# Optimization experiments

Measured on AMD Instinct MI355X. Metric: run time of the kernel, lower is better.

Reference implementation:

```python
import jax, jax.numpy as jnp
import numpy as np

D = 768
B = 32
N = 768


def setup_inputs() -> dict:
    key = jax.random.key(0)
    k1, k2, k3, k4 = jax.random.split(key, 4)
    stdv = 1.0 / np.sqrt(D)
    X = jax.random.normal(k1, (B, N, D), dtype=jnp.float32)
    adj = jax.random.uniform(k2, (B, N, N), dtype=jnp.float32)
    W_l = jax.random.uniform(k3, (D, D), dtype=jnp.float32, minval=-stdv, maxval=stdv)
    W_l1 = jax.random.uniform(k4, (D, D), dtype=jnp.float32, minval=-stdv, maxval=stdv)
    return {"X": X, "adj": adj, "W_l": W_l, "W_l1": W_l1}


def _row_normalize(adj):
    # rowsum^-1 with inf -> 0 (rows summing to zero stay zero)
    rowsum = adj.sum(axis=-1, keepdims=True)  # [B, N, 1]
    r_inv = jnp.where(rowsum == 0, 0.0, 1.0 / rowsum)
    return adj * r_inv


def reference(X, adj, W_l, W_l1):
    # X: [B, N, D], adj: [B, N, N]
    adj_n = _row_normalize(adj)
    e1 = jnp.einsum('bnd,de->bne', X, W_l1)        # message transform
    e11 = jnp.einsum('bnm,bmd->bnd', adj_n, e1)    # aggregate
    X1 = jnp.einsum('bnd,de->bne', X, W_l)         # self transform
    h = X1 + e11
    return jax.nn.leaky_relu(h, negative_slope=0.01)
```

## Files before the change

### kernel.cpp

```cpp
#include <hip/hip_runtime.h>
#include <hip/hip_bf16.h>
#include <cstdint>
#include <cstddef>

#define BN_ROWS 24576
#define DD 768
#define BE (768*768)
#define BM 192
#define BN_T 192
#define BK 32
#define ABUF 12288
#define BUFSZ 24576

typedef __attribute__((ext_vector_type(8))) short bf16x8;
typedef __attribute__((ext_vector_type(4))) float f32x4;
typedef __attribute__((ext_vector_type(8))) unsigned short u16x8;

static __device__ __forceinline__ unsigned short f2bf(float f) {
  unsigned int u = __builtin_bit_cast(unsigned int, f);
  unsigned int lsb = (u >> 16) & 1u;
  u += 0x7fffu + lsb;
  return (unsigned short)(u >> 16);
}

static __device__ __forceinline__ unsigned short f2bfv(float f) {
  __hip_bfloat16 h = __float2bfloat16(f);
  return __builtin_bit_cast(unsigned short, h);
}

static __device__ __forceinline__ bf16x8 cvt8(float4 u, float4 w, float sc) {
  bf16x8 o;
  o[0] = (short)f2bfv(u.x * sc); o[1] = (short)f2bfv(u.y * sc);
  o[2] = (short)f2bfv(u.z * sc); o[3] = (short)f2bfv(u.w * sc);
  o[4] = (short)f2bfv(w.x * sc); o[5] = (short)f2bfv(w.y * sc);
  o[6] = (short)f2bfv(w.z * sc); o[7] = (short)f2bfv(w.w * sc);
  return o;
}


#define PREP_WT 144
#define PREP_FL 288
#define PREP_RS 6144

__global__ __launch_bounds__(256) void prep(const float* __restrict__ adj,
                                            const float* __restrict__ Wl,
                                            const float* __restrict__ Wl1,
                                            float* __restrict__ rinv,
                                            unsigned short* __restrict__ WlT,
                                            unsigned short* __restrict__ Wl1T) {
  __shared__ float tile[64][65];
  const int bid = blockIdx.x;
  if (bid < PREP_WT) {
    const int tr = bid / 12, tc = bid % 12;
    const int c = threadIdx.x & 63, r0 = threadIdx.x >> 6;
    #pragma unroll
    for (int i = 0; i < 16; ++i) {
      int r = r0 + i * 4;
      tile[r][c] = Wl1[(size_t)(tr * 64 + r) * DD + tc * 64 + c];
    }
    __syncthreads();
    #pragma unroll
    for (int i = 0; i < 16; ++i) {
      int r2 = r0 + i * 4;
      Wl1T[(size_t)(tc * 64 + r2) * DD + tr * 64 + c] = f2bf(tile[c][r2]);
    }
  } else if (bid < PREP_WT + PREP_FL) {
    const int b2 = bid - PREP_WT;
    const int wg = b2 * 4 + (threadIdx.x >> 6);
    const int lane = threadIdx.x & 63;
    const int d0 = (wg % 96) * 8;
    const int e = (wg / 96) * 64 + lane;
    u16x8 o;
    #pragma unroll
    for (int j = 0; j < 8; ++j)
      o[j] = f2bf(Wl[(size_t)(d0 + j) * DD + e]);
    const int base = ((e >> 4) * 24 + (d0 >> 5)) * 512
                   + ((e & 15) + (((d0 >> 3) & 3) << 4)) * 8;
    *reinterpret_cast<u16x8*>(WlT + base) = o;
  } else {
    const int rb = bid - (PREP_WT + PREP_FL);
    const int wid = threadIdx.x >> 6, lane = threadIdx.x & 63;
    const int row = rb * 4 + wid;
    const float4* a = reinterpret_cast<const float4*>(adj + (size_t)row * DD);
    float4 v[3];
    float s = 0.f;
    #pragma unroll
    for (int i = 0; i < 3; ++i) {
      v[i] = a[i * 64 + lane];
      s += (v[i].x + v[i].y) + (v[i].z + v[i].w);
    }
    #pragma unroll
    for (int off = 32; off; off >>= 1) s += __shfl_down(s, off);
    if (lane == 0) rinv[row] = (s == 0.f) ? 0.f : 1.f / s;
  }
}

__global__ __launch_bounds__(256, 2) void gemm_e1(
    const float* __restrict__ X,
    const unsigned short* __restrict__ W1T,
    unsigned short* __restrict__ e1T)
{
  __shared__ char smem[2 * BUFSZ];
  constexpr int NT = 24;
  const int tid = threadIdx.x, lane = tid & 63;
  const int wid = tid >> 6;
  const int wr = wid >> 1, wc = wid & 1;

  const int logical = (blockIdx.x & 7) * 64 + (blockIdx.x >> 3);
  const int mt = logical >> 2, nt = logical & 3;
  const int b = mt >> 2;
  const float* Ag = X + (size_t)mt * BM * DD;
  const unsigned short* Bg = W1T + (size_t)nt * BN_T * DD;

  const int r_in = lane >> 2;
  const int s_in = lane & 3;

  float4 aR[3][2];
  auto issueA = [&](int s) {
    int kk = s < NT ? s : 0;
    #pragma unroll
    for (int i = 0; i < 3; ++i) {
      int row = (wid * 3 + i) * 16 + r_in;
      int slot = s_in ^ ((row >> 1) & 3);
      const float4* p = reinterpret_cast<const float4*>(
          Ag + (size_t)row * DD + kk * BK + slot * 8);
      aR[i][0] = p[0];
      aR[i][1] = p[1];
    }
  };
  auto writeA = [&](int s) {
    const int buf = (s & 1) * BUFSZ;
    #pragma unroll
    for (int i = 0; i < 3; ++i)
      *reinterpret_cast<bf16x8*>(smem + buf + (wid * 3 + i) * 1024 + lane * 16) =
          cvt8(aR[i][0], aR[i][1], 1.0f);
  };
  auto issueB = [&](int s) {
    int kk = s < NT ? s : 0;
    const int buf = (s & 1) * BUFSZ + ABUF;
    #pragma unroll
    for (int i = 0; i < 3; ++i) {
      int c = wid * 3 + i;
      int row = c * 16 + r_in;
      int slot = s_in ^ ((row >> 1) & 3);
      const unsigned short* src = Bg + (size_t)row * DD + kk * BK + slot * 8;
      __builtin_amdgcn_global_load_lds(
          (const __attribute__((address_space(1))) void*)src,
          (__attribute__((address_space(3))) void*)(smem + buf + c * 1024),
          16, 0, 0);
    }
  };

  const int ks = lane >> 4;
  auto frag = [&](int off, int row) -> bf16x8 {
    int slot = ks ^ ((row >> 1) & 3);
    return *reinterpret_cast<const bf16x8*>(smem + off + row * 64 + slot * 16);
  };

  f32x4 acc[6][6] = {};
  const int arow = wr * 96 + (lane & 15);
  const int brow = wc * 96 + (lane & 15);

  issueA(0);
  asm volatile("s_waitcnt vmcnt(0)" ::: "memory");
  writeA(0);
  issueB(0);
  issueA(1);
  asm volatile("s_waitcnt lgkmcnt(0)" ::: "memory");
  __builtin_amdgcn_s_barrier();

  for (int t = 0; t < NT; ++t) {
    asm volatile("s_waitcnt vmcnt(6)" ::: "memory");
    __builtin_amdgcn_s_barrier();
    issueB(t + 1);

    const int bufA = (t & 1) * BUFSZ;
    const int bufB = bufA + ABUF;
    bf16x8 a[6], bg[6];
    #pragma unroll
    for (int i = 0; i < 6; ++i) a[i] = frag(bufA, arow + i * 16);
    #pragma unroll
    for (int i = 0; i < 6; ++i) bg[i] = frag(bufB, brow + i * 16);

    __builtin_amdgcn_s_setprio(1);
    #pragma unroll
    for (int ni = 0; ni < 6; ++ni)
      #pragma unroll
      for (int mi = 0; mi < 6; ++mi)
        acc[mi][ni] = __builtin_amdgcn_mfma_f32_16x16x32_bf16(a[mi], bg[ni], acc[mi][ni], 0, 0, 0);
    __builtin_amdgcn_s_setprio(0);

    asm volatile("s_waitcnt vmcnt(3)" ::: "memory");
    writeA(t + 1);
    issueA(t + 2);
    asm volatile("s_waitcnt lgkmcnt(0)" ::: "memory");
  }

  unsigned short* ob = e1T + (size_t)b * BE;
  const int m0 = (mt & 3) * BM + wr * 96 + (lane >> 4) * 4;
  const int l15 = lane & 15;
  #pragma unroll
  for (int mi = 0; mi < 6; ++mi)
    #pragma unroll
    for (int ni = 0; ni < 6; ++ni) {
      int m = m0 + mi * 16;
      int cb = nt * 12 + wc * 6 + ni;
      int fa = (cb * 24 + (m >> 5)) * 512
             + (l15 + (((m >> 3) & 3) << 4)) * 8 + (m & 7);
      f32x4 v = acc[mi][ni];
      ushort4 o;
      o.x = f2bf(v[0]); o.y = f2bf(v[1]); o.z = f2bf(v[2]); o.w = f2bf(v[3]);
      *reinterpret_cast<ushort4*>(ob + fa) = o;
    }
}

__global__ __launch_bounds__(256, 2) void gemm_bg(
    const float* __restrict__ adj,
    const float* __restrict__ X,
    const float* __restrict__ rinv,
    const unsigned short* __restrict__ e1T,
    const unsigned short* __restrict__ WlT,
    float* __restrict__ out)
{
  __shared__ char smem[2 * 12288];
  constexpr int NT = 48;
  const int tid = threadIdx.x, lane = tid & 63;
  const int wid = tid >> 6;
  const int wr = wid >> 1, wc = wid & 1;

  const int logical = (blockIdx.x & 7) * 64 + (blockIdx.x >> 3);
  const int b = logical >> 4;
  const int r = logical & 15;
  const int mt = r >> 2, nt = r & 3;
  const size_t bo = (size_t)b * BE;
  const float* A0 = adj + bo + (size_t)mt * BM * DD;
  const float* A1 = X + (size_t)(b * 768 + mt * BM) * DD;
  const unsigned short* B0 = e1T + bo;
  const unsigned short* B1 = WlT;

  const int r_in = lane >> 2;
  const int s_in = lane & 3;
  const int colblk0 = nt * 12 + wc * 6;

  float rinv3[3];
  #pragma unroll
  for (int i = 0; i < 3; ++i)
    rinv3[i] = rinv[b * 768 + mt * BM + (wid * 3 + i) * 16 + r_in];

  float4 aR[3][2];
  auto issueA = [&](int s) {
    int sc = s < NT ? s : 0;
    const float* base = (sc >= 24) ? A1 : A0;
    int kk = (sc >= 24) ? sc - 24 : sc;
    #pragma unroll
    for (int i = 0; i < 3; ++i) {
      int row = (wid * 3 + i) * 16 + r_in;
      int slot = s_in ^ ((row >> 1) & 3);
      const float4* p = reinterpret_cast<const float4*>(
          base + (size_t)row * DD + kk * BK + slot * 8);
      aR[i][0] = p[0];
      aR[i][1] = p[1];
    }
  };
  auto writeA = [&](int s) {
    int sc = s < NT ? s : 0;
    const bool isAdj = sc < 24;
    const int buf = (s & 1) * 12288;
    #pragma unroll
    for (int i = 0; i < 3; ++i) {
      float scl = isAdj ? rinv3[i] : 1.0f;
      *reinterpret_cast<bf16x8*>(smem + buf + (wid * 3 + i) * 1024 + lane * 16) =
          cvt8(aR[i][0], aR[i][1], scl);
    }
  };
  auto loadB = [&](int s, bf16x8* dst) {
    int sc = s < NT ? s : 0;
    const unsigned short* base = (sc >= 24) ? B1 : B0;
    int kk = (sc >= 24) ? sc - 24 : sc;
    #pragma unroll
    for (int ni = 0; ni < 6; ++ni)
      dst[ni] = *reinterpret_cast<const bf16x8*>(
          base + ((colblk0 + ni) * 24 + kk) * 512 + lane * 8);
  };

  const int ks = lane >> 4;
  auto rdA = [&](int off, int row) -> bf16x8 {
    int slot = ks ^ ((row >> 1) & 3);
    return *reinterpret_cast<const bf16x8*>(smem + off + row * 64 + slot * 16);
  };

  f32x4 acc[6][6] = {};
  const int arow = wr * 96 + (lane & 15);
  bf16x8 bA[6], bB[6];

  auto body = [&](int bufo, bf16x8* bfr) {
    #pragma unroll
    for (int mh = 0; mh < 2; ++mh) {
      bf16x8 a[3];
      #pragma unroll
      for (int i = 0; i < 3; ++i) a[i] = rdA(bufo, arow + mh * 48 + i * 16);
      __builtin_amdgcn_s_setprio(1);
      #pragma unroll
      for (int mi = 0; mi < 3; ++mi)
        #pragma unroll
        for (int ni = 0; ni < 6; ++ni)
          acc[mh * 3 + mi][ni] = __builtin_amdgcn_mfma_f32_16x16x32_bf16(
              a[mi], bfr[ni], acc[mh * 3 + mi][ni], 0, 0, 0);
      __builtin_amdgcn_s_setprio(0);
    }
  };

  issueA(0);
  asm volatile("s_waitcnt vmcnt(0)" ::: "memory");
  writeA(0);
  loadB(0, bA);
  issueA(1);
  asm volatile("s_waitcnt lgkmcnt(0)" ::: "memory");
  __builtin_amdgcn_s_barrier();

  for (int t = 0; t < NT; t += 2) {
    loadB(t + 1, bB);
    body(0, bA);
    asm volatile("s_waitcnt vmcnt(6)" ::: "memory");
    writeA(t + 1);
    issueA(t + 2);
    asm volatile("s_waitcnt lgkmcnt(0)" ::: "memory");
    __builtin_amdgcn_s_barrier();

    loadB(t + 2, bA);
    body(12288, bB);
    asm volatile("s_waitcnt vmcnt(6)" ::: "memory");
    writeA(t + 2);
    issueA(t + 3);
    asm volatile("s_waitcnt lgkmcnt(0)" ::: "memory");
    __builtin_amdgcn_s_barrier();
  }

  float* ob = out + bo;
  const int m0 = mt * BM + wr * 96 + (lane >> 4) * 4;
  const int l15 = lane & 15;
  #pragma unroll
  for (int mi = 0; mi < 6; ++mi)
    #pragma unroll
    for (int ni = 0; ni < 6; ++ni) {
      int m = m0 + mi * 16;
      int n = nt * BN_T + wc * 96 + ni * 16 + l15;
      f32x4 v = acc[mi][ni];
      #pragma unroll
      for (int j = 0; j < 4; ++j) {
        float x = v[j];
        ob[(size_t)(m + j) * DD + n] = x > 0.f ? x : 0.01f * x;
      }
    }
}


extern "C" void kernel_launch(void* const* d_in, const int* in_sizes, int n_in,
                              void* d_out, int out_size, void* d_ws, size_t ws_size,
                              hipStream_t stream) {
  const float* X   = (const float*)d_in[0];
  const float* adj = (const float*)d_in[1];
  const float* Wl  = (const float*)d_in[2];
  const float* Wl1 = (const float*)d_in[3];
  float* out = (float*)d_out;

  char* ws = (char*)d_ws;
  const size_t SZ = (size_t)BN_ROWS * DD * 2;
  unsigned short* e1T  = (unsigned short*)(ws);
  unsigned short* WlT  = (unsigned short*)(ws + SZ);
  unsigned short* Wl1T = (unsigned short*)(ws + SZ + (size_t)BE * 2);
  float* rinv          = (float*)(ws + SZ + 2 * (size_t)BE * 2);

  prep<<<PREP_WT + PREP_FL + PREP_RS, 256, 0, stream>>>(adj, Wl, Wl1, rinv, WlT, Wl1T);
  gemm_e1<<<512, 256, 0, stream>>>(X, Wl1T, e1T);
  gemm_bg<<<512, 256, 0, stream>>>(adj, X, rinv, e1T, WlT, out);
}
```

Baseline: 134.4 us.

## Pre-normalize adj and X to bf16 so main GEMM streams bf16 via LDS DMA

The prep kernel now writes a row-normalized bf16 copy of adj instead of just the reciprocal row sums. gemm_e1 also writes a bf16 copy of X (only the nt==0 tiles). gemm_bg then loads its A operand directly as bf16 with global_load_lds, replacing fp32 loads plus register conversion and the LDS write step. This halves A-operand traffic in the main GEMM and simplifies its pipeline, at the cost of extra writes and reads of the bf16 adj and X buffers in workspace.

```diff
diff --git a/kernel.cpp b/kernel.cpp
--- a/kernel.cpp
+++ b/kernel.cpp
@@ -38,20 +38,44 @@
 }
 
 
-#define PREP_WT 144
-#define PREP_FL 288
-#define PREP_RS 6144
+#define P_AN 3072
+#define P_WT 144
+#define P_FL 288
 
 __global__ __launch_bounds__(256) void prep(const float* __restrict__ adj,
                                             const float* __restrict__ Wl,
                                             const float* __restrict__ Wl1,
-                                            float* __restrict__ rinv,
+                                            unsigned short* __restrict__ adjnb,
                                             unsigned short* __restrict__ WlT,
                                             unsigned short* __restrict__ Wl1T) {
   __shared__ float tile[64][65];
   const int bid = blockIdx.x;
-  if (bid < PREP_WT) {
-    const int tr = bid / 12, tc = bid % 12;
+  if (bid < P_AN) {
+    const int w = threadIdx.x >> 6;
+    const int hl = (threadIdx.x >> 5) & 1;
+    const int l = threadIdx.x & 31;
+    const int row = bid * 8 + w * 2 + hl;
+    const float4* a = reinterpret_cast<const float4*>(adj + (size_t)row * DD);
+    float4 v[6];
+    #pragma unroll
+    for (int i = 0; i < 3; ++i) {
+      int u = l + i * 32;
+      v[2 * i]     = a[u * 2];
+      v[2 * i + 1] = a[u * 2 + 1];
+    }
+    float s = 0.f;
+    #pragma unroll
+    for (int i = 0; i < 6; ++i) s += (v[i].x + v[i].y) + (v[i].z + v[i].w);
+    #pragma unroll
+    for (int off = 16; off; off >>= 1) s += __shfl_xor(s, off);
+    float rinv = (s == 0.f) ? 0.f : 1.f / s;
+    u16x8* o = reinterpret_cast<u16x8*>(adjnb + (size_t)row * DD);
+    #pragma unroll
+    for (int i = 0; i < 3; ++i)
+      o[l + i * 32] = __builtin_bit_cast(u16x8, cvt8(v[2 * i], v[2 * i + 1], rinv));
+  } else if (bid < P_AN + P_WT) {
+    const int tb = bid - P_AN;
+    const int tr = tb / 12, tc = tb % 12;
     const int c = threadIdx.x & 63, r0 = threadIdx.x >> 6;
     #pragma unroll
     for (int i = 0; i < 16; ++i) {
@@ -64,8 +88,8 @@
       int r2 = r0 + i * 4;
       Wl1T[(size_t)(tc * 64 + r2) * DD + tr * 64 + c] = f2bf(tile[c][r2]);
     }
-  } else if (bid < PREP_WT + PREP_FL) {
-    const int b2 = bid - PREP_WT;
+  } else {
+    const int b2 = bid - (P_AN + P_WT);
     const int wg = b2 * 4 + (threadIdx.x >> 6);
     const int lane = threadIdx.x & 63;
     const int d0 = (wg % 96) * 8;
@@ -77,28 +101,14 @@
     const int base = ((e >> 4) * 24 + (d0 >> 5)) * 512
                    + ((e & 15) + (((d0 >> 3) & 3) << 4)) * 8;
     *reinterpret_cast<u16x8*>(WlT + base) = o;
-  } else {
-    const int rb = bid - (PREP_WT + PREP_FL);
-    const int wid = threadIdx.x >> 6, lane = threadIdx.x & 63;
-    const int row = rb * 4 + wid;
-    const float4* a = reinterpret_cast<const float4*>(adj + (size_t)row * DD);
-    float4 v[3];
-    float s = 0.f;
-    #pragma unroll
-    for (int i = 0; i < 3; ++i) {
-      v[i] = a[i * 64 + lane];
-      s += (v[i].x + v[i].y) + (v[i].z + v[i].w);
-    }
-    #pragma unroll
-    for (int off = 32; off; off >>= 1) s += __shfl_down(s, off);
-    if (lane == 0) rinv[row] = (s == 0.f) ? 0.f : 1.f / s;
   }
 }
 
 __global__ __launch_bounds__(256, 2) void gemm_e1(
     const float* __restrict__ X,
     const unsigned short* __restrict__ W1T,
-    unsigned short* __restrict__ e1T)
+    unsigned short* __restrict__ e1T,
+    unsigned short* __restrict__ Xb)
 {
   __shared__ char smem[2 * BUFSZ];
   constexpr int NT = 24;
@@ -134,6 +144,16 @@
     for (int i = 0; i < 3; ++i)
       *reinterpret_cast<bf16x8*>(smem + buf + (wid * 3 + i) * 1024 + lane * 16) =
           cvt8(aR[i][0], aR[i][1], 1.0f);
+  };
+  auto storeXb = [&](int s) {
+    int kk = s < NT ? s : 0;
+    #pragma unroll
+    for (int i = 0; i < 3; ++i) {
+      int row = (wid * 3 + i) * 16 + r_in;
+      int slot = s_in ^ ((row >> 1) & 3);
+      *reinterpret_cast<bf16x8*>(Xb + (size_t)(mt * BM + row) * DD + kk * BK + slot * 8) =
+          cvt8(aR[i][0], aR[i][1], 1.0f);
+    }
   };
   auto issueB = [&](int s) {
     int kk = s < NT ? s : 0;
@@ -192,6 +212,7 @@
 
     asm volatile("s_waitcnt vmcnt(3)" ::: "memory");
     writeA(t + 1);
+    if (nt == 0) storeXb(t + 1);
     issueA(t + 2);
     asm volatile("s_waitcnt lgkmcnt(0)" ::: "memory");
   }
@@ -215,14 +236,13 @@
 }
 
 __global__ __launch_bounds__(256, 2) void gemm_bg(
-    const float* __restrict__ adj,
-    const float* __restrict__ X,
-    const float* __restrict__ rinv,
+    const unsigned short* __restrict__ adjnb,
     const unsigned short* __restrict__ e1T,
+    const unsigned short* __restrict__ Xb,
     const unsigned short* __restrict__ WlT,
     float* __restrict__ out)
 {
-  __shared__ char smem[2 * 12288];
+  __shared__ char smem[24576];
   constexpr int NT = 48;
   const int tid = threadIdx.x, lane = tid & 63;
   const int wid = tid >> 6;
@@ -233,8 +253,8 @@
   const int r = logical & 15;
   const int mt = r >> 2, nt = r & 3;
   const size_t bo = (size_t)b * BE;
-  const float* A0 = adj + bo + (size_t)mt * BM * DD;
-  const float* A1 = X + (size_t)(b * 768 + mt * BM) * DD;
+  const unsigned short* A0 = adjnb + bo + (size_t)mt * BM * DD;
+  const unsigned short* A1 = Xb + bo + (size_t)mt * BM * DD;
   const unsigned short* B0 = e1T + bo;
   const unsigned short* B1 = WlT;
 
@@ -242,37 +262,24 @@
   const int s_in = lane & 3;
   const int colblk0 = nt * 12 + wc * 6;
 
-  float rinv3[3];
-  #pragma unroll
-  for (int i = 0; i < 3; ++i)
-    rinv3[i] = rinv[b * 768 + mt * BM + (wid * 3 + i) * 16 + r_in];
-
-  float4 aR[3][2];
-  auto issueA = [&](int s) {
+  auto stage = [&](int s) {
     int sc = s < NT ? s : 0;
-    const float* base = (sc >= 24) ? A1 : A0;
+    const unsigned short* base = (sc >= 24) ? A1 : A0;
     int kk = (sc >= 24) ? sc - 24 : sc;
-    #pragma unroll
-    for (int i = 0; i < 3; ++i) {
-      int row = (wid * 3 + i) * 16 + r_in;
+    const int buf = (s & 1) * 12288;
+    #pragma unroll
+    for (int i = 0; i < 3; ++i) {
+      int chunk = wid * 3 + i;
+      int row = chunk * 16 + r_in;
       int slot = s_in ^ ((row >> 1) & 3);
-      const float4* p = reinterpret_cast<const float4*>(
-          base + (size_t)row * DD + kk * BK + slot * 8);
-      aR[i][0] = p[0];
-      aR[i][1] = p[1];
-    }
-  };
-  auto writeA = [&](int s) {
-    int sc = s < NT ? s : 0;
-    const bool isAdj = sc < 24;
-    const int buf = (s & 1) * 12288;
-    #pragma unroll
-    for (int i = 0; i < 3; ++i) {
-      float scl = isAdj ? rinv3[i] : 1.0f;
-      *reinterpret_cast<bf16x8*>(smem + buf + (wid * 3 + i) * 1024 + lane * 16) =
-          cvt8(aR[i][0], aR[i][1], scl);
-    }
-  };
+      const unsigned short* src = base + (size_t)row * DD + kk * BK + slot * 8;
+      __builtin_amdgcn_global_load_lds(
+          (const __attribute__((address_space(1))) void*)src,
+          (__attribute__((address_space(3))) void*)(smem + buf + chunk * 1024),
+          16, 0, 0);
+    }
+  };
+
   auto loadB = [&](int s, bf16x8* dst) {
     int sc = s < NT ? s : 0;
     const unsigned short* base = (sc >= 24) ? B1 : B0;
@@ -310,31 +317,18 @@
     }
   };
 
-  issueA(0);
-  asm volatile("s_waitcnt vmcnt(0)" ::: "memory");
-  writeA(0);
-  loadB(0, bA);
-  issueA(1);
-  asm volatile("s_waitcnt lgkmcnt(0)" ::: "memory");
-  __builtin_amdgcn_s_barrier();
-
+  stage(0); loadB(0, bA);
   for (int t = 0; t < NT; t += 2) {
-    loadB(t + 1, bB);
+    asm volatile("s_waitcnt vmcnt(6)" ::: "memory");
+    __builtin_amdgcn_s_barrier();
+    stage(t + 1); loadB(t + 1, bB);
     body(0, bA);
     asm volatile("s_waitcnt vmcnt(6)" ::: "memory");
-    writeA(t + 1);
-    issueA(t + 2);
-    asm volatile("s_waitcnt lgkmcnt(0)" ::: "memory");
     __builtin_amdgcn_s_barrier();
-
-    loadB(t + 2, bA);
+    stage(t + 2); loadB(t + 2, bA);
     body(12288, bB);
-    asm volatile("s_waitcnt vmcnt(6)" ::: "memory");
-    writeA(t + 2);
-    issueA(t + 3);
-    asm volatile("s_waitcnt lgkmcnt(0)" ::: "memory");
-    __builtin_amdgcn_s_barrier();
   }
+  asm volatile("s_waitcnt vmcnt(0)" ::: "memory");
 
   float* ob = out + bo;
   const int m0 = mt * BM + wr * 96 + (lane >> 4) * 4;
@@ -366,12 +360,13 @@
 
   char* ws = (char*)d_ws;
   const size_t SZ = (size_t)BN_ROWS * DD * 2;
-  unsigned short* e1T  = (unsigned short*)(ws);
-  unsigned short* WlT  = (unsigned short*)(ws + SZ);
-  unsigned short* Wl1T = (unsigned short*)(ws + SZ + (size_t)BE * 2);
-  float* rinv          = (float*)(ws + SZ + 2 * (size_t)BE * 2);
-
-  prep<<<PREP_WT + PREP_FL + PREP_RS, 256, 0, stream>>>(adj, Wl, Wl1, rinv, WlT, Wl1T);
-  gemm_e1<<<512, 256, 0, stream>>>(X, Wl1T, e1T);
-  gemm_bg<<<512, 256, 0, stream>>>(adj, X, rinv, e1T, WlT, out);
-}
+  unsigned short* e1T   = (unsigned short*)(ws);
+  unsigned short* adjnb = (unsigned short*)(ws + SZ);
+  unsigned short* Xb    = (unsigned short*)(ws + 2 * SZ);
+  unsigned short* WlT   = (unsigned short*)(ws + 3 * SZ);
+  unsigned short* Wl1T  = (unsigned short*)(ws + 3 * SZ + (size_t)BE * 2);
+
+  prep<<<P_AN + P_WT + P_FL, 256, 0, stream>>>(adj, Wl, Wl1, adjnb, WlT, Wl1T);
+  gemm_e1<<<512, 256, 0, stream>>>(X, Wl1T, e1T, Xb);
+  gemm_bg<<<512, 256, 0, stream>>>(adjnb, e1T, Xb, WlT, out);
+}
```

Result: slower. 157.9 us (+17.5%).

## Stage B operand through LDS via global_load_lds instead of fragment-packed register loads

Applied to the files above, without the earlier changes.

The second GEMM previously read pre-packed MFMA fragments of e1T and WlT directly into registers from global memory. Now e1T and WlT are stored as plain row-major transposes, and the kernel copies B tiles into LDS with global_load_lds in a swizzled layout that matches the A tile, then reads fragments from LDS. The prep kernel is simplified to transpose both weights the same way. The aim is to cut B-operand register pressure and per-wave redundant global reads, at the cost of extra LDS traffic and a per-iteration barrier.

```diff
diff --git a/kernel.cpp b/kernel.cpp
--- a/kernel.cpp
+++ b/kernel.cpp
@@ -22,12 +22,10 @@
   u += 0x7fffu + lsb;
   return (unsigned short)(u >> 16);
 }
-
 static __device__ __forceinline__ unsigned short f2bfv(float f) {
   __hip_bfloat16 h = __float2bfloat16(f);
   return __builtin_bit_cast(unsigned short, h);
 }
-
 static __device__ __forceinline__ bf16x8 cvt8(float4 u, float4 w, float sc) {
   bf16x8 o;
   o[0] = (short)f2bfv(u.x * sc); o[1] = (short)f2bfv(u.y * sc);
@@ -37,10 +35,8 @@
   return o;
 }
 
-
-#define PREP_WT 144
-#define PREP_FL 288
-#define PREP_RS 6144
+#define P_WT 144
+#define P_RS 6144
 
 __global__ __launch_bounds__(256) void prep(const float* __restrict__ adj,
                                             const float* __restrict__ Wl,
@@ -50,35 +46,30 @@
                                             unsigned short* __restrict__ Wl1T) {
   __shared__ float tile[64][65];
   const int bid = blockIdx.x;
-  if (bid < PREP_WT) {
+  if (bid < P_WT) {
     const int tr = bid / 12, tc = bid % 12;
     const int c = threadIdx.x & 63, r0 = threadIdx.x >> 6;
-    #pragma unroll
-    for (int i = 0; i < 16; ++i) {
-      int r = r0 + i * 4;
-      tile[r][c] = Wl1[(size_t)(tr * 64 + r) * DD + tc * 64 + c];
-    }
-    __syncthreads();
-    #pragma unroll
-    for (int i = 0; i < 16; ++i) {
-      int r2 = r0 + i * 4;
-      Wl1T[(size_t)(tc * 64 + r2) * DD + tr * 64 + c] = f2bf(tile[c][r2]);
-    }
-  } else if (bid < PREP_WT + PREP_FL) {
-    const int b2 = bid - PREP_WT;
-    const int wg = b2 * 4 + (threadIdx.x >> 6);
-    const int lane = threadIdx.x & 63;
-    const int d0 = (wg % 96) * 8;
-    const int e = (wg / 96) * 64 + lane;
-    u16x8 o;
-    #pragma unroll
-    for (int j = 0; j < 8; ++j)
-      o[j] = f2bf(Wl[(size_t)(d0 + j) * DD + e]);
-    const int base = ((e >> 4) * 24 + (d0 >> 5)) * 512
-                   + ((e & 15) + (((d0 >> 3) & 3) << 4)) * 8;
-    *reinterpret_cast<u16x8*>(WlT + base) = o;
+    const float* srcs[2] = {Wl, Wl1};
+    unsigned short* dsts[2] = {WlT, Wl1T};
+    #pragma unroll
+    for (int m = 0; m < 2; ++m) {
+      const float* src = srcs[m];
+      #pragma unroll
+      for (int i = 0; i < 16; ++i) {
+        int r = r0 + i * 4;
+        tile[r][c] = src[(size_t)(tr * 64 + r) * DD + tc * 64 + c];
+      }
+      __syncthreads();
+      unsigned short* dst = dsts[m];
+      #pragma unroll
+      for (int i = 0; i < 16; ++i) {
+        int r2 = r0 + i * 4;
+        dst[(size_t)(tc * 64 + r2) * DD + tr * 64 + c] = f2bf(tile[c][r2]);
+      }
+      __syncthreads();
+    }
   } else {
-    const int rb = bid - (PREP_WT + PREP_FL);
+    const int rb = bid - P_WT;
     const int wid = threadIdx.x >> 6, lane = threadIdx.x & 63;
     const int row = rb * 4 + wid;
     const float4* a = reinterpret_cast<const float4*>(adj + (size_t)row * DD);
@@ -204,13 +195,11 @@
     #pragma unroll
     for (int ni = 0; ni < 6; ++ni) {
       int m = m0 + mi * 16;
-      int cb = nt * 12 + wc * 6 + ni;
-      int fa = (cb * 24 + (m >> 5)) * 512
-             + (l15 + (((m >> 3) & 3) << 4)) * 8 + (m & 7);
+      int d = nt * BN_T + wc * 96 + ni * 16 + l15;
       f32x4 v = acc[mi][ni];
       ushort4 o;
       o.x = f2bf(v[0]); o.y = f2bf(v[1]); o.z = f2bf(v[2]); o.w = f2bf(v[3]);
-      *reinterpret_cast<ushort4*>(ob + fa) = o;
+      *reinterpret_cast<ushort4*>(ob + (size_t)d * DD + m) = o;
     }
 }
 
@@ -222,7 +211,7 @@
     const unsigned short* __restrict__ WlT,
     float* __restrict__ out)
 {
-  __shared__ char smem[2 * 12288];
+  __shared__ char smem[2 * BUFSZ];
   constexpr int NT = 48;
   const int tid = threadIdx.x, lane = tid & 63;
   const int wid = tid >> 6;
@@ -235,12 +224,11 @@
   const size_t bo = (size_t)b * BE;
   const float* A0 = adj + bo + (size_t)mt * BM * DD;
   const float* A1 = X + (size_t)(b * 768 + mt * BM) * DD;
-  const unsigned short* B0 = e1T + bo;
-  const unsigned short* B1 = WlT;
+  const unsigned short* Bg0 = e1T + bo + (size_t)nt * BN_T * DD;
+  const unsigned short* Bg1 = WlT + (size_t)nt * BN_T * DD;
 
   const int r_in = lane >> 2;
   const int s_in = lane & 3;
-  const int colblk0 = nt * 12 + wc * 6;
 
   float rinv3[3];
   #pragma unroll
@@ -265,7 +253,7 @@
   auto writeA = [&](int s) {
     int sc = s < NT ? s : 0;
     const bool isAdj = sc < 24;
-    const int buf = (s & 1) * 12288;
+    const int buf = (s & 1) * BUFSZ;
     #pragma unroll
     for (int i = 0; i < 3; ++i) {
       float scl = isAdj ? rinv3[i] : 1.0f;
@@ -273,67 +261,67 @@
           cvt8(aR[i][0], aR[i][1], scl);
     }
   };
-  auto loadB = [&](int s, bf16x8* dst) {
+  auto issueB = [&](int s) {
     int sc = s < NT ? s : 0;
-    const unsigned short* base = (sc >= 24) ? B1 : B0;
+    const unsigned short* base = (sc >= 24) ? Bg1 : Bg0;
     int kk = (sc >= 24) ? sc - 24 : sc;
-    #pragma unroll
-    for (int ni = 0; ni < 6; ++ni)
-      dst[ni] = *reinterpret_cast<const bf16x8*>(
-          base + ((colblk0 + ni) * 24 + kk) * 512 + lane * 8);
+    const int buf = (s & 1) * BUFSZ + ABUF;
+    #pragma unroll
+    for (int i = 0; i < 3; ++i) {
+      int c = wid * 3 + i;
+      int row = c * 16 + r_in;
+      int slot = s_in ^ ((row >> 1) & 3);
+      const unsigned short* src = base + (size_t)row * DD + kk * BK + slot * 8;
+      __builtin_amdgcn_global_load_lds(
+          (const __attribute__((address_space(1))) void*)src,
+          (__attribute__((address_space(3))) void*)(smem + buf + c * 1024),
+          16, 0, 0);
+    }
   };
 
   const int ks = lane >> 4;
-  auto rdA = [&](int off, int row) -> bf16x8 {
+  auto frag = [&](int off, int row) -> bf16x8 {
     int slot = ks ^ ((row >> 1) & 3);
     return *reinterpret_cast<const bf16x8*>(smem + off + row * 64 + slot * 16);
   };
 
   f32x4 acc[6][6] = {};
   const int arow = wr * 96 + (lane & 15);
-  bf16x8 bA[6], bB[6];
-
-  auto body = [&](int bufo, bf16x8* bfr) {
-    #pragma unroll
-    for (int mh = 0; mh < 2; ++mh) {
-      bf16x8 a[3];
-      #pragma unroll
-      for (int i = 0; i < 3; ++i) a[i] = rdA(bufo, arow + mh * 48 + i * 16);
-      __builtin_amdgcn_s_setprio(1);
-      #pragma unroll
-      for (int mi = 0; mi < 3; ++mi)
-        #pragma unroll
-        for (int ni = 0; ni < 6; ++ni)
-          acc[mh * 3 + mi][ni] = __builtin_amdgcn_mfma_f32_16x16x32_bf16(
-              a[mi], bfr[ni], acc[mh * 3 + mi][ni], 0, 0, 0);
-      __builtin_amdgcn_s_setprio(0);
-    }
-  };
+  const int brow = wc * 96 + (lane & 15);
 
   issueA(0);
   asm volatile("s_waitcnt vmcnt(0)" ::: "memory");
   writeA(0);
-  loadB(0, bA);
+  issueB(0);
   issueA(1);
   asm volatile("s_waitcnt lgkmcnt(0)" ::: "memory");
   __builtin_amdgcn_s_barrier();
 
-  for (int t = 0; t < NT; t += 2) {
-    loadB(t + 1, bB);
-    body(0, bA);
+  for (int t = 0; t < NT; ++t) {
     asm volatile("s_waitcnt vmcnt(6)" ::: "memory");
+    __builtin_amdgcn_s_barrier();
+    issueB(t + 1);
+
+    const int bufA = (t & 1) * BUFSZ;
+    const int bufB = bufA + ABUF;
+    bf16x8 a[6], bg[6];
+    #pragma unroll
+    for (int i = 0; i < 6; ++i) a[i] = frag(bufA, arow + i * 16);
+    #pragma unroll
+    for (int i = 0; i < 6; ++i) bg[i] = frag(bufB, brow + i * 16);
+
+    __builtin_amdgcn_s_setprio(1);
+    #pragma unroll
+    for (int ni = 0; ni < 6; ++ni)
+      #pragma unroll
+      for (int mi = 0; mi < 6; ++mi)
+        acc[mi][ni] = __builtin_amdgcn_mfma_f32_16x16x32_bf16(a[mi], bg[ni], acc[mi][ni], 0, 0, 0);
+    __builtin_amdgcn_s_setprio(0);
+
+    asm volatile("s_waitcnt vmcnt(3)" ::: "memory");
     writeA(t + 1);
     issueA(t + 2);
     asm volatile("s_waitcnt lgkmcnt(0)" ::: "memory");
-    __builtin_amdgcn_s_barrier();
-
-    loadB(t + 2, bA);
-    body(12288, bB);
-    asm volatile("s_waitcnt vmcnt(6)" ::: "memory");
-    writeA(t + 2);
-    issueA(t + 3);
-    asm volatile("s_waitcnt lgkmcnt(0)" ::: "memory");
-    __builtin_amdgcn_s_barrier();
   }
 
   float* ob = out + bo;
@@ -371,7 +359,7 @@
   unsigned short* Wl1T = (unsigned short*)(ws + SZ + (size_t)BE * 2);
   float* rinv          = (float*)(ws + SZ + 2 * (size_t)BE * 2);
 
-  prep<<<PREP_WT + PREP_FL + PREP_RS, 256, 0, stream>>>(adj, Wl, Wl1, rinv, WlT, Wl1T);
+  prep<<<P_WT + P_RS, 256, 0, stream>>>(adj, Wl, Wl1, rinv, WlT, Wl1T);
   gemm_e1<<<512, 256, 0, stream>>>(X, Wl1T, e1T);
   gemm_bg<<<512, 256, 0, stream>>>(adj, X, rinv, e1T, WlT, out);
 }
```

New measurement: 152.1 us. 1.13x slower.
